# Performance work log

Hardware: AMD Instinct MI355X
Metric: run time of the kernel (lower is better)

Reference implementation:

```python
import jax, jax.numpy as jnp
import numpy as np

V, H, E = 32000, 1024, 1024
B, S = 64, 128

def setup_inputs() -> dict:
    key = jax.random.key(0)
    ks = jax.random.split(key, 14)
    sc = 0.02
    return {
        "input_batch": jax.random.randint(ks[0], (B, 1), 0, V),
        "prev_h": jax.random.normal(ks[1], (1, B, H), jnp.float32),
        "prev_c": jax.random.normal(ks[2], (1, B, H), jnp.float32),
        "encoder_outputs": jax.random.normal(ks[3], (B, S, H), jnp.float32),
        "lengths": jnp.ones((B,), jnp.int64 if jax.config.read('jax_enable_x64') else jnp.int32),
        "emb": jax.random.normal(ks[4], (V, E), jnp.float32) * sc,
        "attn_w": jax.random.normal(ks[5], (2 * H,), jnp.float32) * sc,
        "attn_b": jax.random.normal(ks[6], (1,), jnp.float32) * sc,
        "W_ih": jax.random.normal(ks[7], (4 * H, E + H), jnp.float32) * sc,
        "W_hh": jax.random.normal(ks[8], (4 * H, H), jnp.float32) * sc,
        "b_ih": jax.random.normal(ks[9], (4 * H,), jnp.float32) * sc,
        "b_hh": jax.random.normal(ks[10], (4 * H,), jnp.float32) * sc,
        "W_out": jax.random.normal(ks[11], (V, H), jnp.float32) * sc,
        "b_out": jax.random.normal(ks[12], (V,), jnp.float32) * sc,
    }

def reference(input_batch, prev_h, prev_c, encoder_outputs, lengths,
              emb, attn_w, attn_b, W_ih, W_hh, b_ih, b_hh, W_out, b_out):
    h0 = prev_h[0]            # [B, H]
    c0 = prev_c[0]            # [B, H]
    x_emb = emb[input_batch[:, 0]]  # [B, E]

    # attention: score[b,s] = concat(h0[b], enc[b,s]) @ attn_w + attn_b
    # (vectorized form of the original per-element Python loop)
    h_part = h0 @ attn_w[:H]                                   # [B]
    e_part = jnp.einsum('bsh,h->bs', encoder_outputs, attn_w[H:])  # [B, S]
    scores = e_part + h_part[:, None] + attn_b[0]
    attn_weights = jax.nn.softmax(scores, axis=-1)             # [B, S]
    context = jnp.einsum('bs,bsh->bh', attn_weights, encoder_outputs)  # [B, H]

    # single-step LSTM cell (torch gate order: i, f, g, o)
    x = jnp.concatenate([x_emb, context], axis=-1)             # [B, E+H]
    gates = x @ W_ih.T + h0 @ W_hh.T + b_ih + b_hh             # [B, 4H]
    i_g, f_g, g_g, o_g = jnp.split(gates, 4, axis=-1)
    c1 = jax.nn.sigmoid(f_g) * c0 + jax.nn.sigmoid(i_g) * jnp.tanh(g_g)
    h1 = jax.nn.sigmoid(o_g) * jnp.tanh(c1)

    # zero-out rows with length == 0
    zmask = (lengths == 0)[:, None]                            # [B, 1]
    h1 = jnp.where(zmask, 0.0, h1)
    c1 = jnp.where(zmask, 0.0, c1)

    logits = h1 @ W_out.T + b_out                              # [B, V]
    logprobs = jax.nn.log_softmax(logits, axis=-1)
    return (logprobs, h1[None], c1[None], attn_weights)
```

## Files before the change

### kernel.cpp

```cpp
#include <hip/hip_runtime.h>
#include <math.h>

constexpr int V = 32000, H = 1024, E = 1024, B = 64, S = 128;
constexpr int KX = 2048;

constexpr long long OUT_H1   = (long long)B * V;
constexpr long long OUT_C1   = OUT_H1 + (long long)B * H;
constexpr long long OUT_ATTN = OUT_C1 + (long long)B * H;

constexpr long long WS_SCORES = 0;
constexpr long long WS_XCAT   = WS_SCORES + (long long)B * S;
constexpr long long WS_PART   = WS_XCAT + (long long)B * KX;
constexpr long long WS_CTXP   = WS_PART + 6LL * B * 4096;
constexpr long long WS_PM     = WS_CTXP + 4LL * B * H;
constexpr long long WS_PL     = WS_PM + 64 * 512;
constexpr long long WS_LC     = WS_PL + 64 * 512;

typedef __attribute__((ext_vector_type(8))) short short8;
typedef __attribute__((ext_vector_type(4))) float f32x4;

__device__ __forceinline__ unsigned short f2bf(float f) {
  unsigned u = __float_as_uint(f);
  u += 0x7FFF + ((u >> 16) & 1);
  return (unsigned short)(u >> 16);
}

__device__ __forceinline__ short8 pack8(float4 a, float4 b) {
  short8 s;
  s[0] = (short)f2bf(a.x); s[1] = (short)f2bf(a.y);
  s[2] = (short)f2bf(a.z); s[3] = (short)f2bf(a.w);
  s[4] = (short)f2bf(b.x); s[5] = (short)f2bf(b.y);
  s[6] = (short)f2bf(b.z); s[7] = (short)f2bf(b.w);
  return s;
}

__device__ __forceinline__ void gemm_body(
    const float* __restrict__ W, int ldw,
    const float* __restrict__ X, int ldx,
    int g0, int k0, int KC,
    float* __restrict__ dst, int ldo, const float* __restrict__ bias,
    float* __restrict__ pm, float* __restrict__ pl) {
  __shared__ __align__(16) unsigned short Wl[64 * 64];
  __shared__ __align__(16) unsigned short Xl[64 * 64];
  __shared__ float pmx[4][64];
  __shared__ float psm[4][64];
  int t = threadIdx.x;
  int lane = t & 63, wid = t >> 6;
  int n = lane & 15, quad = lane >> 4;
  int r0 = t >> 3,          c0 = t & 7;
  int r1 = (t + 256) >> 3,  c1 = (t + 256) & 7;
  int ws0 = r0 * 64 + (c0 ^ (r0 & 7)) * 8;
  int ws1 = r1 * 64 + (c1 ^ (r1 & 7)) * 8;
  f32x4 acc[4] = {{0.f,0.f,0.f,0.f},{0.f,0.f,0.f,0.f},
                  {0.f,0.f,0.f,0.f},{0.f,0.f,0.f,0.f}};
  const float* wp0 = W + (long long)(g0 + r0) * ldw + k0 + c0 * 8;
  const float* wp1 = W + (long long)(g0 + r1) * ldw + k0 + c1 * 8;
  const float* xp0 = X + (long long)r0 * ldx + k0 + c0 * 8;
  const float* xp1 = X + (long long)r1 * ldx + k0 + c1 * 8;
  float4 wa = ((const float4*)wp0)[0], wb = ((const float4*)wp0)[1];
  float4 wc = ((const float4*)wp1)[0], wd = ((const float4*)wp1)[1];
  float4 xa = ((const float4*)xp0)[0], xb = ((const float4*)xp0)[1];
  float4 xc = ((const float4*)xp1)[0], xd = ((const float4*)xp1)[1];

  for (int kt = 0; kt < KC; kt += 64) {
    __syncthreads();
    *(short8*)&Wl[ws0] = pack8(wa, wb);
    *(short8*)&Wl[ws1] = pack8(wc, wd);
    *(short8*)&Xl[ws0] = pack8(xa, xb);
    *(short8*)&Xl[ws1] = pack8(xc, xd);
    __syncthreads();
    if (kt + 64 < KC) {
      int o = kt + 64;
      wa = *(const float4*)(wp0 + o); wb = *(const float4*)(wp0 + o + 4);
      wc = *(const float4*)(wp1 + o); wd = *(const float4*)(wp1 + o + 4);
      xa = *(const float4*)(xp0 + o); xb = *(const float4*)(xp0 + o + 4);
      xc = *(const float4*)(xp1 + o); xd = *(const float4*)(xp1 + o + 4);
    }
#pragma unroll
    for (int kc = 0; kc < 2; ++kc) {
      short8 af = *(const short8*)&Wl[(wid * 16 + n) * 64 +
                                      (((kc * 4 + quad) ^ (n & 7)) * 8)];
#pragma unroll
      for (int nt = 0; nt < 4; ++nt) {
        short8 bf = *(const short8*)&Xl[(nt * 16 + n) * 64 +
                                        (((kc * 4 + quad) ^ (n & 7)) * 8)];
        acc[nt] = __builtin_amdgcn_mfma_f32_16x16x32_bf16(af, bf, acc[nt], 0, 0, 0);
      }
    }
  }
  int gl = wid * 16 + quad * 4;
  float bs[4] = {0.f, 0.f, 0.f, 0.f};
  if (bias) {
#pragma unroll
    for (int r = 0; r < 4; ++r) bs[r] = bias[g0 + gl + r];
  }
  float v[4][4];
#pragma unroll
  for (int nt = 0; nt < 4; ++nt) {
    int b = nt * 16 + n;
#pragma unroll
    for (int r = 0; r < 4; ++r) {
      v[nt][r] = acc[nt][r] + bs[r];
      dst[(long long)b * ldo + g0 + gl + r] = v[nt][r];
    }
  }
  if (pm) {
    float tmax[4];
#pragma unroll
    for (int nt = 0; nt < 4; ++nt) {
      tmax[nt] = fmaxf(fmaxf(v[nt][0], v[nt][1]), fmaxf(v[nt][2], v[nt][3]));
      tmax[nt] = fmaxf(tmax[nt], __shfl_xor(tmax[nt], 16, 64));
      tmax[nt] = fmaxf(tmax[nt], __shfl_xor(tmax[nt], 32, 64));
    }
    if (lane < 16) {
#pragma unroll
      for (int nt = 0; nt < 4; ++nt) pmx[wid][nt * 16 + lane] = tmax[nt];
    }
    __syncthreads();
    float bmax[4], tsum[4];
#pragma unroll
    for (int nt = 0; nt < 4; ++nt) {
      bmax[nt] = fmaxf(fmaxf(pmx[0][nt * 16 + n], pmx[1][nt * 16 + n]),
                       fmaxf(pmx[2][nt * 16 + n], pmx[3][nt * 16 + n]));
      tsum[nt] = __expf(v[nt][0] - bmax[nt]) + __expf(v[nt][1] - bmax[nt]) +
                 __expf(v[nt][2] - bmax[nt]) + __expf(v[nt][3] - bmax[nt]);
      tsum[nt] += __shfl_xor(tsum[nt], 16, 64);
      tsum[nt] += __shfl_xor(tsum[nt], 32, 64);
    }
    if (lane < 16) {
#pragma unroll
      for (int nt = 0; nt < 4; ++nt) psm[wid][nt * 16 + lane] = tsum[nt];
    }
    __syncthreads();
    if (t < 64) {
      float M = fmaxf(fmaxf(pmx[0][t], pmx[1][t]), fmaxf(pmx[2][t], pmx[3][t]));
      float L = psm[0][t] + psm[1][t] + psm[2][t] + psm[3][t];
      pm[t * 512 + blockIdx.x] = M;
      pl[t * 512 + blockIdx.x] = L;
    }
  }
}

__global__ __launch_bounds__(256) void k_gates_mfma(
    const float* __restrict__ W_ih, const float* __restrict__ xcat,
    const float* __restrict__ W_hh, const float* __restrict__ h0,
    float* __restrict__ part) {
  int y = blockIdx.y;
  if (y < 4)
    gemm_body(W_ih, KX, xcat, KX, blockIdx.x * 64, y * 512, 512,
              part + (long long)y * B * 4096, 4096, nullptr, nullptr, nullptr);
  else
    gemm_body(W_hh, H, h0, H, blockIdx.x * 64, (y - 4) * 512, 512,
              part + (long long)y * B * 4096, 4096, nullptr, nullptr, nullptr);
}

__global__ __launch_bounds__(256) void k_logits_mfma(
    const float* __restrict__ W_out, const float* __restrict__ h1,
    float* __restrict__ logits, const float* __restrict__ b_out,
    float* __restrict__ pm, float* __restrict__ pl) {
  gemm_body(W_out, H, h1, H, blockIdx.x * 64, 0, H, logits, V, b_out, pm, pl);
}

__global__ __launch_bounds__(256) void k_attn(
    const float* __restrict__ enc, const float* __restrict__ h0,
    const float* __restrict__ attn_w, const float* __restrict__ attn_b,
    const float* __restrict__ emb, const int* __restrict__ idx,
    float* __restrict__ attn_out, float* __restrict__ xcat) {
  __shared__ float red[256];
  __shared__ float aw[S];
  int b = blockIdx.x, t = threadIdx.x;
  int lane = t & 63, wv = t >> 6;
  const float4* h4  = (const float4*)(h0 + (long long)b * H);
  const float4* w4l = (const float4*)attn_w;
  float4 hv = h4[t], wvv = w4l[t];
  float p = hv.x * wvv.x + hv.y * wvv.y + hv.z * wvv.z + hv.w * wvv.w;
#pragma unroll
  for (int m = 32; m; m >>= 1) p += __shfl_xor(p, m, 64);
  if (lane == 0) red[wv] = p;
  __syncthreads();
  float hp = red[0] + red[1] + red[2] + red[3] + attn_b[0];
  const float4* w4h = (const float4*)(attn_w + H);
  float4 wreg[4];
#pragma unroll
  for (int j = 0; j < 4; ++j) wreg[j] = w4h[lane + 64 * j];
  __syncthreads();
  for (int i = 0; i < 32; ++i) {
    int s = wv * 32 + i;
    const float4* e4 = (const float4*)(enc + (long long)(b * S + s) * H);
    float a = 0.f;
#pragma unroll
    for (int j = 0; j < 4; ++j) {
      float4 e = e4[lane + 64 * j];
      a += e.x * wreg[j].x + e.y * wreg[j].y + e.z * wreg[j].z + e.w * wreg[j].w;
    }
#pragma unroll
    for (int m = 32; m; m >>= 1) a += __shfl_xor(a, m, 64);
    if (lane == 0) aw[s] = a + hp;
  }
  __syncthreads();
  float sc = (t < S) ? aw[t] : -INFINITY;
  red[t] = sc; __syncthreads();
  for (int off = 128; off; off >>= 1) {
    if (t < off) red[t] = fmaxf(red[t], red[t + off]);
    __syncthreads();
  }
  float mx = red[0]; __syncthreads();
  float e = (t < S) ? __expf(sc - mx) : 0.f;
  red[t] = e; __syncthreads();
  for (int off = 128; off; off >>= 1) {
    if (t < off) red[t] += red[t + off];
    __syncthreads();
  }
  float inv = 1.f / red[0];
  if (t < S) {
    float w = e * inv;
    aw[t] = w;
    attn_out[(long long)b * S + t] = w;
  }
  __syncthreads();
  const float4* e4 = (const float4*)(enc + (long long)b * S * H);
  float4 a0 = {0.f,0.f,0.f,0.f}, a1 = {0.f,0.f,0.f,0.f};
#pragma unroll 4
  for (int s = 0; s < S; s += 2) {
    float4 v0 = e4[(long long)s * (H / 4) + t];
    float4 v1 = e4[(long long)(s + 1) * (H / 4) + t];
    float c0 = aw[s], c1 = aw[s + 1];
    a0.x += c0 * v0.x; a0.y += c0 * v0.y; a0.z += c0 * v0.z; a0.w += c0 * v0.w;
    a1.x += c1 * v1.x; a1.y += c1 * v1.y; a1.z += c1 * v1.z; a1.w += c1 * v1.w;
  }
  a0.x += a1.x; a0.y += a1.y; a0.z += a1.z; a0.w += a1.w;
  float4* x4 = (float4*)xcat;
  x4[b * 512 + 256 + t] = a0;
  x4[b * 512 + t] = ((const float4*)emb)[(long long)idx[b] * 256 + t];
}

__global__ __launch_bounds__(256) void k_lstm(
    const float* __restrict__ part, const float* __restrict__ b_ih,
    const float* __restrict__ b_hh, const float* __restrict__ c0,
    const int* __restrict__ lengths,
    float* __restrict__ h1, float* __restrict__ c1) {
  int ft = blockIdx.x * 256 + threadIdx.x;
  int b = ft >> 10, h = ft & 1023;
  float gs[4] = {0.f, 0.f, 0.f, 0.f};
  for (int ks = 0; ks < 6; ++ks) {
    const float* p = part + (long long)(ks * B + b) * 4096;
#pragma unroll
    for (int q = 0; q < 4; ++q) gs[q] += p[q * H + h];
  }
#pragma unroll
  for (int q = 0; q < 4; ++q) gs[q] += b_ih[q * H + h] + b_hh[q * H + h];
  float ig = 1.f / (1.f + expf(-gs[0]));
  float fg = 1.f / (1.f + expf(-gs[1]));
  float gg = tanhf(gs[2]);
  float og = 1.f / (1.f + expf(-gs[3]));
  float c = fg * c0[ft] + ig * gg;
  float hh = og * tanhf(c);
  if (lengths[b] == 0) { c = 0.f; hh = 0.f; }
  h1[ft] = hh; c1[ft] = c;
}

__global__ __launch_bounds__(256) void k_lsm_comb(
    const float* __restrict__ pm, const float* __restrict__ pl,
    float* __restrict__ lc) {
  __shared__ float red[256];
  int b = blockIdx.x, t = threadIdx.x;
  float v0 = pm[b * 512 + t];
  float v1 = (t + 256 < 500) ? pm[b * 512 + t + 256] : -INFINITY;
  red[t] = fmaxf(v0, v1); __syncthreads();
  for (int off = 128; off; off >>= 1) {
    if (t < off) red[t] = fmaxf(red[t], red[t + off]);
    __syncthreads();
  }
  float M = red[0]; __syncthreads();
  float s = pl[b * 512 + t] * __expf(v0 - M);
  if (t + 256 < 500) s += pl[b * 512 + t + 256] * __expf(v1 - M);
  red[t] = s; __syncthreads();
  for (int off = 128; off; off >>= 1) {
    if (t < off) red[t] += red[t + off];
    __syncthreads();
  }
  if (t == 0) lc[b] = M + logf(red[0]);
}

__global__ __launch_bounds__(256) void k_lsm_fin(
    float* __restrict__ logits, const float* __restrict__ lc) {
  int fi = blockIdx.x * 256 + threadIdx.x;
  float4* p = (float4*)logits;
  float4 x = p[fi];
  float c = lc[fi / 8000];
  x.x -= c; x.y -= c; x.z -= c; x.w -= c;
  p[fi] = x;
}

extern "C" void kernel_launch(void* const* d_in, const int* in_sizes, int n_in,
                              void* d_out, int out_size, void* d_ws, size_t ws_size,
                              hipStream_t stream) {
  const int*   input_batch = (const int*)d_in[0];
  const float* prev_h = (const float*)d_in[1];
  const float* prev_c = (const float*)d_in[2];
  const float* enc    = (const float*)d_in[3];
  const int*   lengths= (const int*)d_in[4];
  const float* emb    = (const float*)d_in[5];
  const float* attn_w = (const float*)d_in[6];
  const float* attn_b = (const float*)d_in[7];
  const float* W_ih   = (const float*)d_in[8];
  const float* W_hh   = (const float*)d_in[9];
  const float* b_ih   = (const float*)d_in[10];
  const float* b_hh   = (const float*)d_in[11];
  const float* W_out  = (const float*)d_in[12];
  const float* b_out  = (const float*)d_in[13];

  float* out = (float*)d_out;
  float* ws  = (float*)d_ws;

  float* xcat   = ws + WS_XCAT;
  float* part   = ws + WS_PART;
  float* pm     = ws + WS_PM;
  float* pl     = ws + WS_PL;
  float* lc     = ws + WS_LC;

  float* logits = out;
  float* h1     = out + OUT_H1;
  float* c1     = out + OUT_C1;
  float* attn   = out + OUT_ATTN;

  k_attn<<<dim3(B), 256, 0, stream>>>(enc, prev_h, attn_w, attn_b,
                                      emb, input_batch, attn, xcat);

  k_gates_mfma<<<dim3(64, 6), 256, 0, stream>>>(W_ih, xcat, W_hh, prev_h, part);
  k_lstm<<<dim3(B * H / 256), 256, 0, stream>>>(part, b_ih, b_hh, prev_c,
                                                lengths, h1, c1);

  k_logits_mfma<<<dim3(V / 64), 256, 0, stream>>>(W_out, h1, logits, b_out, pm, pl);

  k_lsm_comb<<<dim3(B), 256, 0, stream>>>(pm, pl, lc);
  k_lsm_fin <<<dim3(B * V / 4 / 256), 256, 0, stream>>>(logits, lc);
}
```

Baseline: 367.3 us.

## Split attention into score, softmax-context, and reduction kernels for more parallelism

The single 64-block attention kernel is replaced by three kernels. One computes per-row encoder scores across 2048 blocks. One runs softmax and a partial context sum over 16 sequence positions each, on a 64x8 grid. The last reduces the 8 partial contexts into xcat. This exposes far more blocks to saturate memory bandwidth on the 32 MB encoder read, at the cost of reading the encoder twice, two extra launches, and a partial-context workspace.

New measurement: 348.4 us. 5.2% less time.

```diff
diff --git a/kernel.cpp b/kernel.cpp
--- a/kernel.cpp
+++ b/kernel.cpp
@@ -12,7 +12,7 @@
 constexpr long long WS_XCAT   = WS_SCORES + (long long)B * S;
 constexpr long long WS_PART   = WS_XCAT + (long long)B * KX;
 constexpr long long WS_CTXP   = WS_PART + 6LL * B * 4096;
-constexpr long long WS_PM     = WS_CTXP + 4LL * B * H;
+constexpr long long WS_PM     = WS_CTXP + 8LL * B * H;
 constexpr long long WS_PL     = WS_PM + 64 * 512;
 constexpr long long WS_LC     = WS_PL + 64 * 512;
 
@@ -161,44 +161,47 @@
   gemm_body(W_out, H, h1, H, blockIdx.x * 64, 0, H, logits, V, b_out, pm, pl);
 }
 
-__global__ __launch_bounds__(256) void k_attn(
-    const float* __restrict__ enc, const float* __restrict__ h0,
-    const float* __restrict__ attn_w, const float* __restrict__ attn_b,
-    const float* __restrict__ emb, const int* __restrict__ idx,
-    float* __restrict__ attn_out, float* __restrict__ xcat) {
+__global__ __launch_bounds__(256) void k_scores(
+    const float* __restrict__ enc, const float* __restrict__ attn_w,
+    float* __restrict__ scores) {
+  int w = (blockIdx.x * 256 + threadIdx.x) >> 6;
+  int lane = threadIdx.x & 63;
+  const float4* e4 = (const float4*)(enc + (long long)w * H);
+  const float4* w4 = (const float4*)(attn_w + H);
+  float acc = 0.f;
+#pragma unroll
+  for (int i = 0; i < 4; ++i) {
+    float4 a = e4[lane + 64 * i];
+    float4 b = w4[lane + 64 * i];
+    acc += a.x * b.x + a.y * b.y + a.z * b.z + a.w * b.w;
+  }
+#pragma unroll
+  for (int m = 32; m; m >>= 1) acc += __shfl_xor(acc, m, 64);
+  if (lane == 0) scores[w] = acc;
+}
+
+__global__ __launch_bounds__(256) void k_smax_ctx(
+    const float* __restrict__ enc, const float* __restrict__ scores,
+    const float* __restrict__ h0, const float* __restrict__ attn_w,
+    const float* __restrict__ attn_b, const float* __restrict__ emb,
+    const int* __restrict__ idx,
+    float* __restrict__ attn_out, float* __restrict__ ctxp,
+    float* __restrict__ xcat) {
   __shared__ float red[256];
   __shared__ float aw[S];
-  int b = blockIdx.x, t = threadIdx.x;
+  int b = blockIdx.x, sq = blockIdx.y, t = threadIdx.x;
   int lane = t & 63, wv = t >> 6;
-  const float4* h4  = (const float4*)(h0 + (long long)b * H);
-  const float4* w4l = (const float4*)attn_w;
-  float4 hv = h4[t], wvv = w4l[t];
-  float p = hv.x * wvv.x + hv.y * wvv.y + hv.z * wvv.z + hv.w * wvv.w;
+  const float4* h4 = (const float4*)(h0 + (long long)b * H);
+  const float4* w4 = (const float4*)attn_w;
+  float4 hv = h4[t], wq = w4[t];
+  float p = hv.x * wq.x + hv.y * wq.y + hv.z * wq.z + hv.w * wq.w;
 #pragma unroll
   for (int m = 32; m; m >>= 1) p += __shfl_xor(p, m, 64);
   if (lane == 0) red[wv] = p;
   __syncthreads();
   float hp = red[0] + red[1] + red[2] + red[3] + attn_b[0];
-  const float4* w4h = (const float4*)(attn_w + H);
-  float4 wreg[4];
-#pragma unroll
-  for (int j = 0; j < 4; ++j) wreg[j] = w4h[lane + 64 * j];
   __syncthreads();
-  for (int i = 0; i < 32; ++i) {
-    int s = wv * 32 + i;
-    const float4* e4 = (const float4*)(enc + (long long)(b * S + s) * H);
-    float a = 0.f;
-#pragma unroll
-    for (int j = 0; j < 4; ++j) {
-      float4 e = e4[lane + 64 * j];
-      a += e.x * wreg[j].x + e.y * wreg[j].y + e.z * wreg[j].z + e.w * wreg[j].w;
-    }
-#pragma unroll
-    for (int m = 32; m; m >>= 1) a += __shfl_xor(a, m, 64);
-    if (lane == 0) aw[s] = a + hp;
-  }
-  __syncthreads();
-  float sc = (t < S) ? aw[t] : -INFINITY;
+  float sc = (t < S) ? (scores[b * S + t] + hp) : -INFINITY;
   red[t] = sc; __syncthreads();
   for (int off = 128; off; off >>= 1) {
     if (t < off) red[t] = fmaxf(red[t], red[t + off]);
@@ -215,23 +218,40 @@
   if (t < S) {
     float w = e * inv;
     aw[t] = w;
-    attn_out[(long long)b * S + t] = w;
+    if (sq == 0) attn_out[(long long)b * S + t] = w;
   }
   __syncthreads();
-  const float4* e4 = (const float4*)(enc + (long long)b * S * H);
-  float4 a0 = {0.f,0.f,0.f,0.f}, a1 = {0.f,0.f,0.f,0.f};
+  const float4* e4 = (const float4*)enc;
+  float4 a0 = {0.f, 0.f, 0.f, 0.f}, a1 = {0.f, 0.f, 0.f, 0.f};
+  int s0 = sq * 16;
 #pragma unroll 4
-  for (int s = 0; s < S; s += 2) {
-    float4 v0 = e4[(long long)s * (H / 4) + t];
-    float4 v1 = e4[(long long)(s + 1) * (H / 4) + t];
-    float c0 = aw[s], c1 = aw[s + 1];
+  for (int s = 0; s < 16; s += 2) {
+    float4 v0 = e4[(long long)(b * S + s0 + s) * (H / 4) + t];
+    float4 v1 = e4[(long long)(b * S + s0 + s + 1) * (H / 4) + t];
+    float c0 = aw[s0 + s], c1 = aw[s0 + s + 1];
     a0.x += c0 * v0.x; a0.y += c0 * v0.y; a0.z += c0 * v0.z; a0.w += c0 * v0.w;
     a1.x += c1 * v1.x; a1.y += c1 * v1.y; a1.z += c1 * v1.z; a1.w += c1 * v1.w;
   }
   a0.x += a1.x; a0.y += a1.y; a0.z += a1.z; a0.w += a1.w;
-  float4* x4 = (float4*)xcat;
-  x4[b * 512 + 256 + t] = a0;
-  x4[b * 512 + t] = ((const float4*)emb)[(long long)idx[b] * 256 + t];
+  ((float4*)ctxp)[(long long)(sq * B + b) * (H / 4) + t] = a0;
+  if (sq == 0) {
+    ((float4*)xcat)[b * 512 + t] =
+        ((const float4*)emb)[(long long)idx[b] * 256 + t];
+  }
+}
+
+__global__ __launch_bounds__(256) void k_xcat_ctx(
+    const float* __restrict__ ctxp, float* __restrict__ xcat) {
+  int ft = blockIdx.x * 256 + threadIdx.x;
+  int b = ft >> 8, hq = ft & 255;
+  const float4* c4 = (const float4*)ctxp;
+  float4 ctx = c4[(0 * B + b) * 256 + hq];
+#pragma unroll
+  for (int sq = 1; sq < 8; ++sq) {
+    float4 v = c4[(sq * B + b) * 256 + hq];
+    ctx.x += v.x; ctx.y += v.y; ctx.z += v.z; ctx.w += v.w;
+  }
+  ((float4*)xcat)[b * 512 + 256 + hq] = ctx;
 }
 
 __global__ __launch_bounds__(256) void k_lstm(
@@ -313,8 +333,10 @@
   float* out = (float*)d_out;
   float* ws  = (float*)d_ws;
 
+  float* scores = ws + WS_SCORES;
   float* xcat   = ws + WS_XCAT;
   float* part   = ws + WS_PART;
+  float* ctxp   = ws + WS_CTXP;
   float* pm     = ws + WS_PM;
   float* pl     = ws + WS_PL;
   float* lc     = ws + WS_LC;
@@ -324,8 +346,11 @@
   float* c1     = out + OUT_C1;
   float* attn   = out + OUT_ATTN;
 
-  k_attn<<<dim3(B), 256, 0, stream>>>(enc, prev_h, attn_w, attn_b,
-                                      emb, input_batch, attn, xcat);
+  k_scores  <<<dim3(B * S / 4), 256, 0, stream>>>(enc, attn_w, scores);
+  k_smax_ctx<<<dim3(B, 8),      256, 0, stream>>>(enc, scores, prev_h, attn_w,
+                                                  attn_b, emb, input_batch,
+                                                  attn, ctxp, xcat);
+  k_xcat_ctx<<<dim3(B * 256 / 256), 256, 0, stream>>>(ctxp, xcat);
 
   k_gates_mfma<<<dim3(64, 6), 256, 0, stream>>>(W_ih, xcat, W_hh, prev_h, part);
   k_lstm<<<dim3(B * H / 256), 256, 0, stream>>>(part, b_ih, b_hh, prev_c,
```
